# Kernel tuning notes

Measured on AMD Instinct MI355X. Metric: run time of the kernel, lower is better.

## Reference

```python
import jax, jax.numpy as jnp
import numpy as np

B, D_BYTES, R, S, NSEG, OUT_DIM = 8, 128, 4096, 32768, 1024, 512
D_BITS = 8 * D_BYTES  # 1024


def setup_inputs() -> dict:
    key = jax.random.key(0)
    ks = jax.random.split(key, 9)
    u8 = lambda k, shape: jax.random.randint(k, shape, 0, 256, dtype=jnp.int32).astype(jnp.uint8)
    Q = u8(ks[0], (B, D_BYTES))
    Q_ok = u8(ks[1], (B, D_BYTES))
    refs = u8(ks[2], (R, D_BYTES))
    ok_pos = u8(ks[3], (R, D_BYTES))
    ref2seg = jax.random.randint(ks[4], (S,), 0, R, dtype=jnp.int32)
    segments = jnp.sort(jax.random.randint(ks[5], (S,), 0, NSEG, dtype=jnp.int32))
    W_o = jax.random.normal(ks[6], (D_BITS, OUT_DIM), dtype=jnp.float32) * (1.0 / np.sqrt(D_BITS))
    b_o = jnp.zeros((OUT_DIM,), dtype=jnp.float32)
    return {"Q": Q, "Q_ok": Q_ok, "refs": refs, "ok_pos": ok_pos,
            "ref2seg": ref2seg, "segments": segments, "N": NSEG,
            "W_o": W_o, "b_o": b_o}


def reference(Q, Q_ok, refs, ok_pos, ref2seg, segments, N, W_o, b_o):
    # values: unpack packed reference bit-sequences once: (R, d_bits) uint8
    values = jnp.unpackbits(refs, axis=1)

    def per_query(q, q_ok):
        # popcount sequence similarity, normalized by non-gap overlap length
        ok = jnp.sum(jax.lax.population_count(jnp.bitwise_and(q_ok, ok_pos)), axis=1)      # (R,)
        match = jnp.sum(jax.lax.population_count(jnp.bitwise_and(q, refs)), axis=1)        # (R,)
        dists = match / ok                                                                  # (R,) float32
        # numerically-stable segment softmax over ragged neighborhoods
        applied = jnp.take(dists, ref2seg)                                                  # (S,)
        mx = jnp.take(jax.ops.segment_max(applied, segments, num_segments=N), segments)
        e = applied - mx
        norm = jnp.take(jnp.log(jax.ops.segment_sum(jnp.exp(e), segments, num_segments=N)), segments)
        scores = jnp.exp(e - norm)                                                          # (S,)
        # gather values along edges, weight, scatter-sum into segments
        av = jnp.take(values, ref2seg, axis=0) * scores[:, None]                            # (S, d_bits)
        return jax.ops.segment_sum(av, segments, num_segments=N)                            # (N, d_bits)

    V = jax.vmap(per_query)(Q, Q_ok)        # (B, N, d_bits)
    return V @ W_o + b_o                     # (B, N, out_dim)
```

## Files before the change

kernel.cpp:

```cpp
#include <hip/hip_runtime.h>

#define B_Q   8
#define DB    128
#define R_REF 4096
#define S_EDGE 32768
#define NSEG  1024
#define DBITS 1024
#define OUTD  512

#define NB_GEMM 512
#define NB_DIST 2048
#define NB_BOUNDS 4
#define TILE_E 256

typedef __bf16 bf16_t;
typedef bf16_t bf16x8 __attribute__((ext_vector_type(8)));
typedef float  f32x4  __attribute__((ext_vector_type(4)));
typedef unsigned int u32;

__device__ inline unsigned short f2bf(float f){
  unsigned int u = __builtin_bit_cast(unsigned int, f);
  u = (u + 0x7fffu + ((u >> 16) & 1u)) >> 16;
  return (unsigned short)u;
}

__global__ __launch_bounds__(256) void k_front(const float* __restrict__ W,
                                               const int* __restrict__ refs,
                                               const int* __restrict__ Q,
                                               const int* __restrict__ Qok,
                                               const int* __restrict__ okpos,
                                               float* __restrict__ distsT,
                                               const int* __restrict__ segments,
                                               int* __restrict__ segstart,
                                               unsigned short* __restrict__ U){
  __shared__ unsigned short AS[2 * 8192];
  __shared__ unsigned short BS[2 * 8192];
  const int bid = blockIdx.x;
  const int tid = threadIdx.x;

  if (bid < NB_GEMM){
    const int tn = (bid & 7) * 64, tm = (bid >> 3) * 64;
    const int w = tid >> 6, l = tid & 63;
    const int wm = (w & 1) * 32, wn = (w >> 1) * 32;
    const int lr = l & 15, kq = l >> 4;

    f32x4 acc[2][2] = {};
    int cur = 0;

    #define STAGE_A(buf, K0)                                                               \
      do {                                                                                 \
        int row = tid >> 2, j0 = (tid & 3) * 4;                                            \
        int4 rv = *(const int4*)(refs + (size_t)(tm + row) * DB + (K0)/8 + j0);            \
        const int rx = row & 15;                                                           \
        int vv[4] = {rv.x, rv.y, rv.z, rv.w};                                              \
        _Pragma("unroll")                                                                  \
        for (int j = 0; j < 4; ++j){                                                       \
          u32 v = (u32)vv[j];                                                              \
          uint4 o;                                                                         \
          u32* wp = (u32*)&o;                                                              \
          _Pragma("unroll")                                                                \
          for (int i2 = 0; i2 < 4; ++i2){                                                  \
            u32 b0 = (v >> (7 - 2*i2)) & 1u;                                               \
            u32 b1 = (v >> (6 - 2*i2)) & 1u;                                               \
            wp[i2] = b0 * 0x3F80u | ((b1 * 0x3F80u) << 16);                                \
          }                                                                                \
          int lch = (j0 + j) ^ rx;                                                         \
          *(uint4*)(AS + (buf)*8192 + row*128 + lch*8) = o;                                \
        }                                                                                  \
      } while (0)

    #define STAGE_BW(buf, K0)                                                              \
      do {                                                                                 \
        _Pragma("unroll")                                                                  \
        for (int c = 0; c < 4; ++c){                                                       \
          int idx = c * 256 + tid;                                                         \
          int kpair = idx >> 4, oq = idx & 15;                                             \
          int k = (K0) + kpair * 2;                                                        \
          float4 w0 = *(const float4*)(W + (size_t)k * OUTD + tn + oq * 4);                \
          float4 w1 = *(const float4*)(W + (size_t)(k + 1) * OUTD + tn + oq * 4);          \
          int krel = kpair * 2;                                                            \
          int gch = krel >> 3, kb = krel & 7;                                              \
          float wa0[4] = {w0.x, w0.y, w0.z, w0.w};                                         \
          float wa1[4] = {w1.x, w1.y, w1.z, w1.w};                                         \
          _Pragma("unroll")                                                                \
          for (int j = 0; j < 4; ++j){                                                     \
            int row = oq * 4 + j;                                                          \
            int ch = gch ^ (row & 15);                                                     \
            u32 val = (u32)f2bf(wa0[j]) | ((u32)f2bf(wa1[j]) << 16);                       \
            *(u32*)(BS + (buf)*8192 + row*128 + ch*8 + kb) = val;                          \
          }                                                                                \
        }                                                                                  \
      } while (0)

    STAGE_BW(0, 0);
    STAGE_A(0, 0);
    __syncthreads();

    for (int s = 0; s < 8; ++s){
      if (s < 7){ STAGE_BW(cur ^ 1, (s + 1) * 128); STAGE_A(cur ^ 1, (s + 1) * 128); }
      #pragma unroll
      for (int kk = 0; kk < 4; ++kk){
        bf16x8 af[2], bfr[2];
        #pragma unroll
        for (int m = 0; m < 2; ++m){
          int row = wm + m*16 + lr;
          int ch  = (kk*4 + kq) ^ (row & 15);
          af[m] = __builtin_bit_cast(bf16x8, *(const uint4*)(AS + cur*8192 + row*128 + ch*8));
        }
        #pragma unroll
        for (int n = 0; n < 2; ++n){
          int row = wn + n*16 + lr;
          int ch  = (kk*4 + kq) ^ (row & 15);
          bfr[n] = __builtin_bit_cast(bf16x8, *(const uint4*)(BS + cur*8192 + row*128 + ch*8));
        }
        #pragma unroll
        for (int m = 0; m < 2; ++m)
          #pragma unroll
          for (int n = 0; n < 2; ++n)
            acc[m][n] = __builtin_amdgcn_mfma_f32_16x16x32_bf16(af[m], bfr[n], acc[m][n], 0, 0, 0);
      }
      __syncthreads();
      cur ^= 1;
    }
    #undef STAGE_A
    #undef STAGE_BW

    #pragma unroll
    for (int n = 0; n < 2; ++n)
      #pragma unroll
      for (int m = 0; m < 2; ++m){
        int row = tm + wm + m*16 + kq*4;
        int col = tn + wn + n*16 + lr;
        #pragma unroll
        for (int q = 0; q < 4; ++q)
          U[(size_t)(row + q) * OUTD + col] = f2bf(acc[m][n][q]);
      }
  } else if (bid < NB_GEMM + NB_DIST){
    const int w = tid >> 6, l = tid & 63;
    const int base = (bid - NB_GEMM) * 16 + w * 4;
    const int b = base >> 12;
    const int q0 = Q[b*DB + l],   q1 = Q[b*DB + 64 + l];
    const int a0 = Qok[b*DB + l], a1 = Qok[b*DB + 64 + l];
    #pragma unroll
    for (int i = 0; i < 4; ++i){
      int r = (base + i) & 4095;
      int f0 = refs[r*DB + l], f1 = refs[r*DB + 64 + l];
      int p0 = okpos[r*DB + l],p1 = okpos[r*DB + 64 + l];
      int m = __popc(q0 & f0) + __popc(q1 & f1);
      int o = __popc(a0 & p0) + __popc(a1 & p1);
      int v = m | (o << 16);
      #pragma unroll
      for (int off = 32; off; off >>= 1) v += __shfl_down(v, off);
      if (l == 0) distsT[r * 8 + b] = (float)(v & 0xffff) / (float)(v >> 16);
    }
  } else {
    int n = (bid - NB_GEMM - NB_DIST) * 256 + tid;
    int lo = 0, hi = S_EDGE;
    #pragma unroll 1
    while (lo < hi){ int mid = (lo + hi) >> 1; if (segments[mid] < n) lo = mid + 1; else hi = mid; }
    segstart[n] = lo;
    if (n == 0) segstart[NSEG] = S_EDGE;
  }
}

__global__ __launch_bounds__(256) void k_scat(const float* __restrict__ distsT,
                                              const int* __restrict__ ref2seg,
                                              const int* __restrict__ segstart,
                                              const unsigned short* __restrict__ U,
                                              const float* __restrict__ bo,
                                              float* __restrict__ out){
  __shared__ float mbs[8], ibs[8];
  __shared__ float scl[TILE_E * 8];
  __shared__ int   rix[TILE_E];
  const int n = blockIdx.x;
  const int t = threadIdx.x;

  const int start = segstart[n], end = segstart[n + 1];

  const float b0c = bo[2*t], b1c = bo[2*t + 1];
  float* op = out + (size_t)n * OUTD + 2*t;

  if (start >= end){
    #pragma unroll
    for (int j = 0; j < 8; ++j){
      op[(size_t)j * NSEG * OUTD]     = b0c;
      op[(size_t)j * NSEG * OUTD + 1] = b1c;
    }
    return;
  }

  if (t < 64){
    const int sb = t >> 3, es = t & 7;
    float m = -1e30f, s = 0.f;
    for (int e = start + es; e < end; e += 8){
      float d = distsT[ref2seg[e] * 8 + sb];
      float mn = fmaxf(m, d);
      s = s * __expf(m - mn) + __expf(d - mn);
      m = mn;
    }
    #pragma unroll
    for (int msk = 1; msk < 8; msk <<= 1){
      float mo = __shfl_xor(m, msk), so = __shfl_xor(s, msk);
      float mn = fmaxf(m, mo);
      s = s * __expf(m - mn) + so * __expf(mo - mn);
      m = mn;
    }
    if (es == 0){ mbs[sb] = m; ibs[sb] = 1.0f / s; }
  }
  __syncthreads();

  float acc[8][2];
  #pragma unroll
  for (int j = 0; j < 8; ++j){ acc[j][0] = 0.f; acc[j][1] = 0.f; }

  for (int e0 = start; e0 < end; e0 += TILE_E){
    const int cnt = min(TILE_E, end - e0);
    for (int i = t; i < cnt * 8; i += 256){
      int e = e0 + (i >> 3), b = i & 7;
      int r = ref2seg[e];
      if (b == 0) rix[i >> 3] = r;
      scl[i] = __expf(distsT[r*8 + b] - mbs[b]) * ibs[b];
    }
    __syncthreads();

    #pragma unroll 4
    for (int e = 0; e < cnt; ++e){
      int r = rix[e];
      float4 s0 = *(const float4*)(scl + e*8);
      float4 s1 = *(const float4*)(scl + e*8 + 4);
      u32 uu = *(const u32*)(U + ((size_t)r << 9) + 2*t);
      float ux = __builtin_bit_cast(float, uu << 16);
      float uy = __builtin_bit_cast(float, uu & 0xffff0000u);
      float ss[8] = {s0.x, s0.y, s0.z, s0.w, s1.x, s1.y, s1.z, s1.w};
      #pragma unroll
      for (int j = 0; j < 8; ++j){
        acc[j][0] += ss[j] * ux;
        acc[j][1] += ss[j] * uy;
      }
    }
    __syncthreads();
  }

  #pragma unroll
  for (int j = 0; j < 8; ++j){
    op[(size_t)j * NSEG * OUTD]     = acc[j][0] + b0c;
    op[(size_t)j * NSEG * OUTD + 1] = acc[j][1] + b1c;
  }
}

extern "C" void kernel_launch(void* const* d_in, const int* in_sizes, int n_in,
                              void* d_out, int out_size, void* d_ws, size_t ws_size,
                              hipStream_t stream) {
  const int*   Q        = (const int*)d_in[0];
  const int*   Qok      = (const int*)d_in[1];
  const int*   refs     = (const int*)d_in[2];
  const int*   okpos    = (const int*)d_in[3];
  const int*   ref2seg  = (const int*)d_in[4];
  const int*   segments = (const int*)d_in[5];
  const float* W        = (const float*)d_in[7];
  const float* bo       = (const float*)d_in[8];
  float* out = (float*)d_out;

  char* ws = (char*)d_ws;
  float*          distsT   = (float*)(ws + (1u<<20));
  int*            segstart = (int*)(ws + (1u<<20) + (160u<<10));
  unsigned short* U        = (unsigned short*)(ws + (11u<<20));

  k_front<<<NB_GEMM + NB_DIST + NB_BOUNDS, 256, 0, stream>>>(W, refs, Q, Qok, okpos,
                                                             distsT, segments, segstart, U);
  k_scat <<<NSEG, 256, 0, stream>>>(distsT, ref2seg, segstart, U, bo, out);
}
```

Baseline: 48.78 us.

## Pre-convert W to transposed bf16 and stage it via global_load_lds

Adds a separate kernel that transposes W once and converts it to bf16 in workspace. The GEMM blocks then stage the B tile with direct global-to-LDS 16-byte loads instead of loading fp32, converting and scattering 4-byte writes in every block. This removes redundant conversion work across the 64 row-tiles and shrinks B-tile traffic. The cost is an extra kernel launch and a write plus re-read of the bf16 copy of W.

```diff
diff --git a/kernel.cpp b/kernel.cpp
--- a/kernel.cpp
+++ b/kernel.cpp
@@ -24,15 +24,34 @@
   return (unsigned short)u;
 }
 
-__global__ __launch_bounds__(256) void k_front(const float* __restrict__ W,
-                                               const int* __restrict__ refs,
-                                               const int* __restrict__ Q,
-                                               const int* __restrict__ Qok,
-                                               const int* __restrict__ okpos,
-                                               float* __restrict__ distsT,
-                                               const int* __restrict__ segments,
-                                               int* __restrict__ segstart,
-                                               unsigned short* __restrict__ U){
+__device__ __forceinline__ void gl_lds16(const unsigned short* g, unsigned short* l){
+  __builtin_amdgcn_global_load_lds((const __attribute__((address_space(1))) u32*)g,
+                                   (__attribute__((address_space(3))) u32*)l, 16, 0, 0);
+}
+
+__global__ __launch_bounds__(256) void k_wconv(const float* __restrict__ W,
+                                               unsigned short* __restrict__ WT){
+  __shared__ float tile[64][65];
+  const int k0 = (blockIdx.x & 15) * 64, o0 = (blockIdx.x >> 4) * 64;
+  const int tr = threadIdx.x >> 6, tc = threadIdx.x & 63;
+  #pragma unroll
+  for (int i = 0; i < 16; ++i)
+    tile[tr + i*4][tc] = W[(size_t)(k0 + tr + i*4) * OUTD + o0 + tc];
+  __syncthreads();
+  #pragma unroll
+  for (int i = 0; i < 16; ++i)
+    WT[(size_t)(o0 + tr + i*4) * DBITS + k0 + tc] = f2bf(tile[tc][tr + i*4]);
+}
+
+__global__ __launch_bounds__(256) void k_mid(const int* __restrict__ refs,
+                                             const unsigned short* __restrict__ WT,
+                                             unsigned short* __restrict__ U,
+                                             const int* __restrict__ Q,
+                                             const int* __restrict__ Qok,
+                                             const int* __restrict__ okpos,
+                                             float* __restrict__ distsT,
+                                             const int* __restrict__ segments,
+                                             int* __restrict__ segstart){
   __shared__ unsigned short AS[2 * 8192];
   __shared__ unsigned short BS[2 * 8192];
   const int bid = blockIdx.x;
@@ -46,6 +65,18 @@
 
     f32x4 acc[2][2] = {};
     int cur = 0;
+
+    #define STAGE_B(buf, K0)                                                               \
+      do {                                                                                 \
+        _Pragma("unroll")                                                                  \
+        for (int c = 0; c < 4; ++c){                                                       \
+          int idx = c * 256 + tid;                                                         \
+          int row = idx >> 4, ch = idx & 15;                                               \
+          int gch = ch ^ (row & 15);                                                       \
+          gl_lds16(WT + (size_t)(tn + row) * DBITS + (K0) + gch*8,                         \
+                   BS + (buf)*8192 + row*128 + ch*8);                                      \
+        }                                                                                  \
+      } while (0)
 
     #define STAGE_A(buf, K0)                                                               \
       do {                                                                                 \
@@ -69,35 +100,12 @@
         }                                                                                  \
       } while (0)
 
-    #define STAGE_BW(buf, K0)                                                              \
-      do {                                                                                 \
-        _Pragma("unroll")                                                                  \
-        for (int c = 0; c < 4; ++c){                                                       \
-          int idx = c * 256 + tid;                                                         \
-          int kpair = idx >> 4, oq = idx & 15;                                             \
-          int k = (K0) + kpair * 2;                                                        \
-          float4 w0 = *(const float4*)(W + (size_t)k * OUTD + tn + oq * 4);                \
-          float4 w1 = *(const float4*)(W + (size_t)(k + 1) * OUTD + tn + oq * 4);          \
-          int krel = kpair * 2;                                                            \
-          int gch = krel >> 3, kb = krel & 7;                                              \
-          float wa0[4] = {w0.x, w0.y, w0.z, w0.w};                                         \
-          float wa1[4] = {w1.x, w1.y, w1.z, w1.w};                                         \
-          _Pragma("unroll")                                                                \
-          for (int j = 0; j < 4; ++j){                                                     \
-            int row = oq * 4 + j;                                                          \
-            int ch = gch ^ (row & 15);                                                     \
-            u32 val = (u32)f2bf(wa0[j]) | ((u32)f2bf(wa1[j]) << 16);                       \
-            *(u32*)(BS + (buf)*8192 + row*128 + ch*8 + kb) = val;                          \
-          }                                                                                \
-        }                                                                                  \
-      } while (0)
-
-    STAGE_BW(0, 0);
+    STAGE_B(0, 0);
     STAGE_A(0, 0);
     __syncthreads();
 
     for (int s = 0; s < 8; ++s){
-      if (s < 7){ STAGE_BW(cur ^ 1, (s + 1) * 128); STAGE_A(cur ^ 1, (s + 1) * 128); }
+      if (s < 7){ STAGE_B(cur ^ 1, (s + 1) * 128); STAGE_A(cur ^ 1, (s + 1) * 128); }
       #pragma unroll
       for (int kk = 0; kk < 4; ++kk){
         bf16x8 af[2], bfr[2];
@@ -123,7 +131,7 @@
       cur ^= 1;
     }
     #undef STAGE_A
-    #undef STAGE_BW
+    #undef STAGE_B
 
     #pragma unroll
     for (int n = 0; n < 2; ++n)
@@ -262,11 +270,13 @@
   float* out = (float*)d_out;
 
   char* ws = (char*)d_ws;
+  unsigned short* WT       = (unsigned short*)ws;
   float*          distsT   = (float*)(ws + (1u<<20));
   int*            segstart = (int*)(ws + (1u<<20) + (160u<<10));
   unsigned short* U        = (unsigned short*)(ws + (11u<<20));
 
-  k_front<<<NB_GEMM + NB_DIST + NB_BOUNDS, 256, 0, stream>>>(W, refs, Q, Qok, okpos,
-                                                             distsT, segments, segstart, U);
+  k_wconv<<<128, 256, 0, stream>>>(W, WT);
+  k_mid  <<<NB_GEMM + NB_DIST + NB_BOUNDS, 256, 0, stream>>>(refs, WT, U, Q, Qok, okpos,
+                                                             distsT, segments, segstart);
   k_scat <<<NSEG, 256, 0, stream>>>(distsT, ref2seg, segstart, U, bo, out);
 }
```

Result: no change. 48.18 us (-1.2%).
